# Kernel optimization log

Measured on AMD Instinct MI355X. Metric: run time of the kernel, lower is better.

The kernel has to match this reference:

```python
import jax, jax.numpy as jnp
import numpy as np

H = 2048
E = 8
K = 2
INTER = 2048
T = 2048


def setup_inputs() -> dict:
    key = jax.random.key(0)
    k1, k2, k3 = jax.random.split(key, 3)
    hidden_4d = jax.random.normal(k1, (1, 1, T, H), dtype=jnp.float32)
    # learned per-expert fused gate+up projection: [1, E, H, 2*inter]
    gate_up_proj = jax.random.normal(k2, (1, E, H, INTER * 2), dtype=jnp.float32) * 0.02
    # binary (expert, token) dispatch mask: on average K of E experts active per token
    sparsity = (jax.random.uniform(k3, (1, E, T, 1)) < (K / E)).astype(jnp.float32)
    return {"hidden_4d": hidden_4d, "gate_up_proj": gate_up_proj, "sparsity": sparsity}


def reference(hidden_4d, gate_up_proj, sparsity):
    # sparse_matmul semantics: per-expert GEMM of tokens against expert weight
    # blocks, with output blocks zeroed (skipped) where the sparsity mask is 0.
    # hidden_4d: [1, 1, T, H]; gate_up_proj: [1, E, H, F]; sparsity: [1, E, T, 1]
    # out[a, e, t, f] = mask[a, e, t] * sum_h hidden[a, 0, t, h] * W[a, e, h, f]
    out = jnp.einsum("abth,aehf->aetf", hidden_4d, gate_up_proj) * sparsity
    return out.sum()
```

## Files before the change

kernel.cpp:

```cpp
#include <hip/hip_runtime.h>

#define H_DIM 2048
#define E_DIM 8
#define T_DIM 2048
#define F_DIM 4096
#define ROWS (E_DIM * H_DIM)
#define TCHUNK 128
#define TCHUNKS 16
#define A_BLOCKS 32
#define RS_BLOCKS 1024
#define RS_WAVES (RS_BLOCKS * 4)
#define ROWS_PER_WAVE (ROWS / RS_WAVES)

typedef float f32x4 __attribute__((ext_vector_type(4)));


__global__ __launch_bounds__(256) void fused_compute(
    const float* __restrict__ hidden,
    const float* __restrict__ W,
    const float* __restrict__ mask,
    float* __restrict__ ws,
    float* __restrict__ out) {
  float* Bsum = ws;
  float* Ap   = ws + ROWS;
  int bid = blockIdx.x;
  int tid = threadIdx.x;

  if (bid < A_BLOCKS) {
    if (bid == 0 && tid == 0) out[0] = 0.f;

    int hb = bid & 1;
    int tc = bid >> 1;
    int t0 = tc * TCHUNK;
    int h4 = hb * 1024 + tid * 4;

    __shared__ float m_lds[E_DIM][TCHUNK];
    #pragma unroll
    for (int i = 0; i < (E_DIM * TCHUNK) / 256; ++i) {
      int idx = i * 256 + tid;
      int e = idx >> 7, tt = idx & 127;
      m_lds[e][tt] = mask[e * T_DIM + t0 + tt];
    }
    __syncthreads();

    f32x4 acc[E_DIM];
    #pragma unroll
    for (int e = 0; e < E_DIM; ++e) acc[e] = (f32x4)0.f;
    #pragma unroll 2
    for (int t = 0; t < TCHUNK; ++t) {
      f32x4 hv = *(const f32x4*)(hidden + (size_t)(t0 + t) * H_DIM + h4);
      #pragma unroll
      for (int e = 0; e < E_DIM; ++e)
        acc[e] += hv * m_lds[e][t];
    }
    #pragma unroll
    for (int e = 0; e < E_DIM; ++e)
      *(f32x4*)(Ap + (size_t)tc * ROWS + e * H_DIM + h4) = acc[e];
  } else {
    int wv   = ((bid - A_BLOCKS) << 2) | (tid >> 6);
    int lane = tid & 63;
    float s[ROWS_PER_WAVE];
    #pragma unroll
    for (int rr = 0; rr < ROWS_PER_WAVE; ++rr) {
      int row = wv + rr * RS_WAVES;
      const f32x4* rp = (const f32x4*)(W + (size_t)row * F_DIM);
      f32x4 a = (f32x4)0.f;
      #pragma unroll
      for (int i = 0; i < 16; ++i)
        a += rp[lane + (i << 6)];
      s[rr] = (a.x + a.y) + (a.z + a.w);
    }
    #pragma unroll
    for (int off = 32; off > 0; off >>= 1) {
      #pragma unroll
      for (int rr = 0; rr < ROWS_PER_WAVE; ++rr)
        s[rr] += __shfl_down(s[rr], off, 64);
    }
    if (lane == 0) {
      #pragma unroll
      for (int rr = 0; rr < ROWS_PER_WAVE; ++rr)
        Bsum[wv + rr * RS_WAVES] = s[rr];
    }
  }
}

__global__ __launch_bounds__(1024) void dot_kernel(const float* __restrict__ ws,
                                                   float* __restrict__ out) {
  const f32x4* B4 = (const f32x4*)ws;
  const f32x4* A4 = (const f32x4*)(ws + ROWS);
  int i = blockIdx.x * 1024 + threadIdx.x;

  f32x4 a = (f32x4)0.f;
  #pragma unroll
  for (int c = 0; c < TCHUNKS; ++c)
    a += A4[(size_t)c * (ROWS / 4) + i];
  f32x4 b = B4[i];
  float s = (a.x * b.x + a.y * b.y) + (a.z * b.z + a.w * b.w);

  #pragma unroll
  for (int off = 32; off > 0; off >>= 1)
    s += __shfl_down(s, off, 64);

  __shared__ float red[16];
  int wave = threadIdx.x >> 6;
  int lane = threadIdx.x & 63;
  if (lane == 0) red[wave] = s;
  __syncthreads();
  if (threadIdx.x == 0) {
    float r = 0.f;
    #pragma unroll
    for (int w = 0; w < 16; ++w) r += red[w];
    atomicAdd(out, r);
  }
}

extern "C" void kernel_launch(void* const* d_in, const int* in_sizes, int n_in,
                              void* d_out, int out_size, void* d_ws, size_t ws_size,
                              hipStream_t stream) {
  const float* hidden = (const float*)d_in[0];
  const float* W      = (const float*)d_in[1];
  const float* mask   = (const float*)d_in[2];
  float* out = (float*)d_out;
  float* ws  = (float*)d_ws;

  fused_compute<<<A_BLOCKS + RS_BLOCKS, 256, 0, stream>>>(hidden, W, mask, ws, out);
  dot_kernel<<<4, 1024, 0, stream>>>(ws, out);
}
```

Baseline: 387.5 us.

## Fuse masked token-sum and weight row-sum into single per-block dot kernel

Replaces the two-kernel scheme (a fused A/B partial-sum kernel plus a separate dot-reduction kernel through workspace) with one kernel. Each block owns one expert and a 16-row H chunk: it computes the masked token sum over all T for its 16 columns of hidden, row-sums the matching W rows, and atomically adds the dot product. This removes the workspace round-trip and the second launch, and adds a memset for the output. In exchange, each of the 1024 blocks rereads a slice of hidden over all T (hidden is reread once per expert), which adds redundant traffic that is mostly expected to hit in cache.

```diff
diff --git a/kernel.cpp b/kernel.cpp
--- a/kernel.cpp
+++ b/kernel.cpp
@@ -4,114 +4,89 @@
 #define E_DIM 8
 #define T_DIM 2048
 #define F_DIM 4096
-#define ROWS (E_DIM * H_DIM)
-#define TCHUNK 128
-#define TCHUNKS 16
-#define A_BLOCKS 32
-#define RS_BLOCKS 1024
-#define RS_WAVES (RS_BLOCKS * 4)
-#define ROWS_PER_WAVE (ROWS / RS_WAVES)
+#define NBLK  1024
+#define HCHUNK 16
 
 typedef float f32x4 __attribute__((ext_vector_type(4)));
 
-
-__global__ __launch_bounds__(256) void fused_compute(
+__global__ __launch_bounds__(256, 4) void moe_dot(
     const float* __restrict__ hidden,
     const float* __restrict__ W,
     const float* __restrict__ mask,
-    float* __restrict__ ws,
     float* __restrict__ out) {
-  float* Bsum = ws;
-  float* Ap   = ws + ROWS;
-  int bid = blockIdx.x;
-  int tid = threadIdx.x;
+  const int tid = threadIdx.x;
+  const int bid = blockIdx.x;
+  const int e   = bid >> 7;
+  const int h0  = (bid & 127) * HCHUNK;
 
-  if (bid < A_BLOCKS) {
-    if (bid == 0 && tid == 0) out[0] = 0.f;
+  __shared__ float m_lds[T_DIM];
+  __shared__ f32x4 redA[4][4];
+  __shared__ float A_val[HCHUNK];
+  __shared__ float wsum[4];
 
-    int hb = bid & 1;
-    int tc = bid >> 1;
-    int t0 = tc * TCHUNK;
-    int h4 = hb * 1024 + tid * 4;
+  {
+    const f32x4* m4 = (const f32x4*)(mask + (size_t)e * T_DIM);
+    f32x4* l4 = (f32x4*)m_lds;
+    l4[tid]       = m4[tid];
+    l4[tid + 256] = m4[tid + 256];
+  }
+  __syncthreads();
 
-    __shared__ float m_lds[E_DIM][TCHUNK];
+  {
+    const int hq  = tid & 3;
+    const int ttg = tid >> 2;
+    const float* hp = hidden + h0 + (hq << 2);
+    f32x4 acc = (f32x4)0.f;
+    #pragma unroll 8
+    for (int k = 0; k < 32; ++k) {
+      int t = ttg + (k << 6);
+      f32x4 hv = *(const f32x4*)(hp + (size_t)t * H_DIM);
+      acc += hv * m_lds[t];
+    }
     #pragma unroll
-    for (int i = 0; i < (E_DIM * TCHUNK) / 256; ++i) {
-      int idx = i * 256 + tid;
-      int e = idx >> 7, tt = idx & 127;
-      m_lds[e][tt] = mask[e * T_DIM + t0 + tt];
+    for (int off = 4; off <= 32; off <<= 1) {
+      acc.x += __shfl_down(acc.x, off, 64);
+      acc.y += __shfl_down(acc.y, off, 64);
+      acc.z += __shfl_down(acc.z, off, 64);
+      acc.w += __shfl_down(acc.w, off, 64);
+    }
+    const int wave = tid >> 6;
+    const int lane = tid & 63;
+    if (lane < 4) redA[wave][lane] = acc;
+    __syncthreads();
+    if (tid < 4) {
+      f32x4 a = redA[0][tid] + redA[1][tid] + redA[2][tid] + redA[3][tid];
+      ((f32x4*)A_val)[tid] = a;
     }
     __syncthreads();
+  }
 
-    f32x4 acc[E_DIM];
-    #pragma unroll
-    for (int e = 0; e < E_DIM; ++e) acc[e] = (f32x4)0.f;
-    #pragma unroll 2
-    for (int t = 0; t < TCHUNK; ++t) {
-      f32x4 hv = *(const f32x4*)(hidden + (size_t)(t0 + t) * H_DIM + h4);
-      #pragma unroll
-      for (int e = 0; e < E_DIM; ++e)
-        acc[e] += hv * m_lds[e][t];
-    }
-    #pragma unroll
-    for (int e = 0; e < E_DIM; ++e)
-      *(f32x4*)(Ap + (size_t)tc * ROWS + e * H_DIM + h4) = acc[e];
-  } else {
-    int wv   = ((bid - A_BLOCKS) << 2) | (tid >> 6);
-    int lane = tid & 63;
-    float s[ROWS_PER_WAVE];
-    #pragma unroll
-    for (int rr = 0; rr < ROWS_PER_WAVE; ++rr) {
-      int row = wv + rr * RS_WAVES;
-      const f32x4* rp = (const f32x4*)(W + (size_t)row * F_DIM);
-      f32x4 a = (f32x4)0.f;
-      #pragma unroll
-      for (int i = 0; i < 16; ++i)
-        a += rp[lane + (i << 6)];
-      s[rr] = (a.x + a.y) + (a.z + a.w);
-    }
-    #pragma unroll
-    for (int off = 32; off > 0; off >>= 1) {
-      #pragma unroll
-      for (int rr = 0; rr < ROWS_PER_WAVE; ++rr)
-        s[rr] += __shfl_down(s[rr], off, 64);
-    }
-    if (lane == 0) {
-      #pragma unroll
-      for (int rr = 0; rr < ROWS_PER_WAVE; ++rr)
-        Bsum[wv + rr * RS_WAVES] = s[rr];
-    }
+  const int wave = tid >> 6;
+  const int lane = tid & 63;
+  const int rl   = wave << 2;
+  const f32x4* rp = (const f32x4*)(W + ((size_t)e * H_DIM + h0 + rl) * F_DIM);
+
+  f32x4 a0 = (f32x4)0.f, a1 = (f32x4)0.f, a2 = (f32x4)0.f, a3 = (f32x4)0.f;
+  #pragma unroll
+  for (int i = 0; i < 16; ++i) {
+    int idx = lane + (i << 6);
+    a0 += rp[idx];
+    a1 += rp[idx + 1024];
+    a2 += rp[idx + 2048];
+    a3 += rp[idx + 3072];
   }
-}
-
-__global__ __launch_bounds__(1024) void dot_kernel(const float* __restrict__ ws,
-                                                   float* __restrict__ out) {
-  const f32x4* B4 = (const f32x4*)ws;
-  const f32x4* A4 = (const f32x4*)(ws + ROWS);
-  int i = blockIdx.x * 1024 + threadIdx.x;
-
-  f32x4 a = (f32x4)0.f;
-  #pragma unroll
-  for (int c = 0; c < TCHUNKS; ++c)
-    a += A4[(size_t)c * (ROWS / 4) + i];
-  f32x4 b = B4[i];
-  float s = (a.x * b.x + a.y * b.y) + (a.z * b.z + a.w * b.w);
+  float dot = ((a0.x + a0.y) + (a0.z + a0.w)) * A_val[rl]
+            + ((a1.x + a1.y) + (a1.z + a1.w)) * A_val[rl + 1]
+            + ((a2.x + a2.y) + (a2.z + a2.w)) * A_val[rl + 2]
+            + ((a3.x + a3.y) + (a3.z + a3.w)) * A_val[rl + 3];
 
   #pragma unroll
   for (int off = 32; off > 0; off >>= 1)
-    s += __shfl_down(s, off, 64);
-
-  __shared__ float red[16];
-  int wave = threadIdx.x >> 6;
-  int lane = threadIdx.x & 63;
-  if (lane == 0) red[wave] = s;
+    dot += __shfl_down(dot, off, 64);
+  if (lane == 0) wsum[wave] = dot;
   __syncthreads();
-  if (threadIdx.x == 0) {
-    float r = 0.f;
-    #pragma unroll
-    for (int w = 0; w < 16; ++w) r += red[w];
-    atomicAdd(out, r);
-  }
+  if (tid == 0)
+    atomicAdd(out, (wsum[0] + wsum[1]) + (wsum[2] + wsum[3]));
 }
 
 extern "C" void kernel_launch(void* const* d_in, const int* in_sizes, int n_in,
@@ -121,8 +96,7 @@
   const float* W      = (const float*)d_in[1];
   const float* mask   = (const float*)d_in[2];
   float* out = (float*)d_out;
-  float* ws  = (float*)d_ws;
 
-  fused_compute<<<A_BLOCKS + RS_BLOCKS, 256, 0, stream>>>(hidden, W, mask, ws, out);
-  dot_kernel<<<4, 1024, 0, stream>>>(ws, out);
+  hipMemsetAsync(d_out, 0, sizeof(float), stream);
+  moe_dot<<<NBLK, 256, 0, stream>>>(hidden, W, mask, out);
 }
```

Result: no change. 382.5 us (-1.3%).
